# Optimization experiments

Hardware: AMD Instinct MI355X
Metric: run time of the kernel (lower is better)

The kernel has to match this reference:

```python
import jax, jax.numpy as jnp
import numpy as np

N_WIRES = 8
DIM = 2 ** N_WIRES  # 256 amplitudes
# PauliZ sign table: Z_SIGNS[w, i] = +1 if bit w of basis index i is 0 else -1
_bits = (np.arange(DIM)[None, :] >> (N_WIRES - 1 - np.arange(N_WIRES))[:, None]) & 1
Z_SIGNS = jnp.asarray(1.0 - 2.0 * _bits, dtype=jnp.float32)  # [8, 256]


def quantum_project(t, theta):
    """Batched 8-wire circuit: RX(x_w) encoder + trainable RX(theta_w) (RX gates on the
    same wire compose additively), then CNOT ring, then <Z_w> for each wire.
    t: [B, S, E] -> returns [B, S, H, 8]."""
    B, S, E = t.shape
    H = E // N_WIRES
    ang = (t.reshape(B, S, H, N_WIRES) + theta) * 0.5  # RX(a)RX(b)=RX(a+b)
    q0 = jnp.cos(ang).astype(jnp.complex64)
    q1 = (-1j * jnp.sin(ang)).astype(jnp.complex64)
    # Build product state |psi> = \otimes_w [cos(a_w/2), -i sin(a_w/2)] -> [B,S,H,256]
    state = jnp.ones((B, S, H, 1), jnp.complex64)
    for w in range(N_WIRES):
        qb = jnp.stack([q0[..., w], q1[..., w]], axis=-1)  # [B,S,H,2]
        state = (state[..., :, None] * qb[..., None, :]).reshape(B, S, H, -1)
    state = state.reshape((B, S, H) + (2,) * N_WIRES)  # wire w on axis 3+w
    # CNOT chain 0->1,...,6->7 then ring-closing 7->0
    for cw, tw in [(w, w + 1) for w in range(N_WIRES - 1)] + [(N_WIRES - 1, 0)]:
        s0 = jax.lax.index_in_dim(state, 0, axis=3 + cw, keepdims=True)
        s1 = jnp.flip(jax.lax.index_in_dim(state, 1, axis=3 + cw, keepdims=True), axis=3 + tw)
        state = jnp.concatenate([s0, s1], axis=3 + cw)
    amps = state.reshape(B, S, H, DIM)
    probs = amps.real * amps.real + amps.imag * amps.imag  # [B,S,H,256] float32
    return jnp.einsum('bshd,wd->bshw', probs, Z_SIGNS)  # <Z_w> per wire


def setup_inputs() -> dict:
    key = jax.random.key(0)
    kx, kq, kk, kv, ko, kt = jax.random.split(key, 6)
    B, S, E = 16, 512, 64
    scale = 1.0 / np.sqrt(E)
    return {
        'x': jax.random.normal(kx, (B, S, E), dtype=jnp.float32),
        'Wq': jax.random.normal(kq, (E, E), dtype=jnp.float32) * scale,
        'Wk': jax.random.normal(kk, (E, E), dtype=jnp.float32) * scale,
        'Wv': jax.random.normal(kv, (E, E), dtype=jnp.float32) * scale,
        'Wo': jax.random.normal(ko, (E, E), dtype=jnp.float32) * scale,
        'theta': jax.random.uniform(kt, (N_WIRES,), dtype=jnp.float32, minval=0.0, maxval=2.0 * np.pi),
    }


def reference(x, Wq, Wk, Wv, Wo, theta):
    B, S, E = x.shape
    q = quantum_project(x @ Wq.T, theta)  # [B,S,H,8]
    k = quantum_project(x @ Wk.T, theta)
    v = quantum_project(x @ Wv.T, theta)
    # NOTE: original code never transposes heads to dim 1, so attention mixes HEADS
    # per token: scores [B,S,H,H]. Faithfully reproduced. d_k = 8.
    scores = jnp.einsum('bsiw,bsjw->bsij', q, k) / jnp.float32(np.sqrt(N_WIRES))
    attn = jax.nn.softmax(scores, axis=-1)  # dropout is identity in eval
    out = jnp.einsum('bsij,bsjw->bsiw', attn, v)  # [B,S,H,8]
    # original: out.transpose(1,2).contiguous().view(B,-1,E) -> scrambled layout
    out = out.transpose(0, 2, 1, 3).reshape(B, -1, E)
    return out @ Wo.T
```

## Files before the change

### kernel.cpp

```cpp
#include <hip/hip_runtime.h>


#define WT  4096
#define SPS 66
#define SCS 17

__device__ __forceinline__ float rl(float v, int l) {
    return __int_as_float(__builtin_amdgcn_readlane(__float_as_int(v), l));
}

#define DPP_SHR_STEP(d, j, sh)                                                 \
    {                                                                          \
        float _t = __int_as_float(__builtin_amdgcn_update_dpp(                 \
            0x3f800000, __float_as_int(d), 0x110 + sh, 0xf, 0xf, false));      \
        d *= ((j) >= (sh)) ? _t : 1.0f;                                        \
    }

__device__ __forceinline__ float fastcos(float x) { return __cosf(x); }

__global__ __launch_bounds__(256, 2)
void qattn_fused(const float* __restrict__ xg,
                 const float* __restrict__ wqg, const float* __restrict__ wkg,
                 const float* __restrict__ wvg, const float* __restrict__ wog,
                 const float* __restrict__ thg,
                 float* __restrict__ outg)
{
    __shared__ float sWt[3 * WT];
    __shared__ float sP[4 * 3 * 4 * SPS];
    __shared__ float sScr[64 * SCS];

    const int tid  = threadIdx.x;
    const int lane = tid & 63;
    const int wg   = tid >> 6;
    const int j    = lane & 7;
    const int b    = blockIdx.x >> 5;
    const int grp  = blockIdx.x & 31;

    {
        const float* gm[3] = {wqg, wkg, wvg};
        #pragma unroll
        for (int m = 0; m < 3; ++m) {
            #pragma unroll
            for (int r = 0; r < 4; ++r) {
                const int g = tid + 256 * r;
                const float4 v = ((const float4*)gm[m])[g];
                const int e = g >> 4, kq = g & 15;
                const int c0 = (2 * e + 4 * kq) & 127;
                const int c1 = (c0 + 2) & 127;
                *(float2*)&sWt[m * WT + 256 * kq + c0]       = make_float2(v.x, v.y);
                *(float2*)&sWt[m * WT + 256 * kq + 128 + c1] = make_float2(v.z, v.w);
            }
        }
    }
    float xr[4];
    {
        const float* xb = xg + ((size_t)(b * 512 + grp * 16 + wg * 4)) * 64 + lane;
        xr[0] = xb[0]; xr[1] = xb[64]; xr[2] = xb[128]; xr[3] = xb[192];
    }
    const float thf = thg[j];
    __syncthreads();

    {
        float acc[3][4];
        #pragma unroll
        for (int m = 0; m < 3; ++m)
            #pragma unroll
            for (int t = 0; t < 4; ++t) acc[m][t] = 0.f;

        #pragma unroll 8
        for (int kk = 0; kk < 32; ++kk) {
            const int col = (2 * lane + 2 * kk) & 127;
            const float2 wq = *(const float2*)&sWt[0 * WT + kk * 128 + col];
            const float2 wk = *(const float2*)&sWt[1 * WT + kk * 128 + col];
            const float2 wv = *(const float2*)&sWt[2 * WT + kk * 128 + col];
            #pragma unroll
            for (int t = 0; t < 4; ++t) {
                const float x0 = rl(xr[t], 2 * kk);
                const float x1 = rl(xr[t], 2 * kk + 1);
                acc[0][t] = fmaf(wq.x, x0, fmaf(wq.y, x1, acc[0][t]));
                acc[1][t] = fmaf(wk.x, x0, fmaf(wk.y, x1, acc[1][t]));
                acc[2][t] = fmaf(wv.x, x0, fmaf(wv.y, x1, acc[2][t]));
            }
        }
        #pragma unroll
        for (int m = 0; m < 3; ++m) {
            #pragma unroll
            for (int t = 0; t < 4; ++t) {
                const float c = fastcos(acc[m][t] + thf);
                float d = c;
                DPP_SHR_STEP(d, j, 1)
                DPP_SHR_STEP(d, j, 2)
                DPP_SHR_STEP(d, j, 4)
                float ex = (j == 0) ? 1.0f : c;
                DPP_SHR_STEP(ex, j, 1)
                DPP_SHR_STEP(ex, j, 2)
                DPP_SHR_STEP(ex, j, 4)
                const int base = (((wg * 3 + m) * 4 + t)) * SPS + lane;
                if (j > 0)  sP[base]     = d;
                if (j == 7) sP[base - 7] = ex;
            }
        }
    }
    __syncthreads();

    if (wg < 2) {
        const int tg = wg * 8 + (lane >> 3);
        const int i  = lane & 7;
        const int qb = (((tg >> 2) * 3 + 0) * 4 + (tg & 3)) * SPS;
        const int kb = qb + 4 * SPS;
        const int vb = qb + 8 * SPS;
        float q[8];
        #pragma unroll
        for (int c = 0; c < 4; ++c)
            *(float2*)&q[2 * c] = *(const float2*)&sP[qb + 8 * i + 2 * c];
        float p[8];
        float sum = 0.f;
        #pragma unroll
        for (int jj = 0; jj < 8; ++jj) {
            float kv[8];
            #pragma unroll
            for (int c = 0; c < 4; ++c)
                *(float2*)&kv[2 * c] = *(const float2*)&sP[kb + 8 * jj + 2 * c];
            float s = q[0] * kv[0];
            #pragma unroll
            for (int w = 1; w < 8; ++w) s = fmaf(q[w], kv[w], s);
            p[jj] = __expf(s * 0.35355339059327373f);
            sum += p[jj];
        }
        const float rinv = 1.0f / sum;
        float o[8];
        #pragma unroll
        for (int w = 0; w < 8; ++w) o[w] = 0.f;
        #pragma unroll
        for (int jj = 0; jj < 8; ++jj) {
            float vv[8];
            #pragma unroll
            for (int c = 0; c < 4; ++c)
                *(float2*)&vv[2 * c] = *(const float2*)&sP[vb + 8 * jj + 2 * c];
            const float a = p[jj] * rinv;
            #pragma unroll
            for (int w = 0; w < 8; ++w) o[w] = fmaf(a, vv[w], o[w]);
        }
        const int rho = i * 2 + (tg >> 3);
        const int cb  = 8 * (tg & 7);
        #pragma unroll
        for (int w = 0; w < 8; ++w) sScr[(cb + w) * SCS + rho] = o[w];
    } else {
        const int lt = tid & 127;
        #pragma unroll
        for (int r = 0; r < 8; ++r) {
            const int g = lt + 128 * r;
            const float4 v = ((const float4*)wog)[g];
            const int e = g >> 4, kq = g & 15;
            const int c0 = (2 * e + 4 * kq) & 127;
            const int c1 = (c0 + 2) & 127;
            *(float2*)&sWt[256 * kq + c0]       = make_float2(v.x, v.y);
            *(float2*)&sWt[256 * kq + 128 + c1] = make_float2(v.z, v.w);
        }
    }
    __syncthreads();

    {
        float wo[64];
        #pragma unroll
        for (int kk = 0; kk < 32; ++kk) {
            const int col = (2 * lane + 2 * kk) & 127;
            const float2 w2 = *(const float2*)&sWt[kk * 128 + col];
            wo[2 * kk] = w2.x; wo[2 * kk + 1] = w2.y;
        }
        #pragma unroll
        for (int rr = 0; rr < 4; ++rr) {
            const int rho = wg * 4 + rr;
            const float sv = sScr[lane * SCS + rho];
            float y0 = 0.f, y1 = 0.f, y2 = 0.f, y3 = 0.f;
            #pragma unroll
            for (int k = 0; k < 64; k += 4) {
                y0 = fmaf(wo[k],     rl(sv, k),     y0);
                y1 = fmaf(wo[k + 1], rl(sv, k + 1), y1);
                y2 = fmaf(wo[k + 2], rl(sv, k + 2), y2);
                y3 = fmaf(wo[k + 3], rl(sv, k + 3), y3);
            }
            const float y = (y0 + y1) + (y2 + y3);
            const int head = rho >> 1, oct = rho & 1;
            outg[((size_t)(b * 512 + head * 64 + grp * 2 + oct)) * 64 + lane] = y;
        }
    }
}

extern "C" void kernel_launch(void* const* d_in, const int* in_sizes, int n_in,
                              void* d_out, int out_size, void* d_ws, size_t ws_size,
                              hipStream_t stream) {
    const float* x  = (const float*)d_in[0];
    const float* wq = (const float*)d_in[1];
    const float* wk = (const float*)d_in[2];
    const float* wv = (const float*)d_in[3];
    const float* wo = (const float*)d_in[4];
    const float* th = (const float*)d_in[5];
    float* out = (float*)d_out;
    qattn_fused<<<dim3(512), dim3(256), 0, stream>>>(x, wq, wk, wv, wo, th, out);
}
```

Measured before the change: 73.50 us.

## Broadcast activations via LDS float4 reads instead of readlane, pad weight layout

Stages the block's x tile in shared memory and reads it as broadcast float4 loads, replacing per-element readlane broadcasts in the QKV projection. The output projection does the same, reading attention rows from a row-major padded scratch buffer. Weights are stored transposed with a padded row stride to avoid bank conflicts, replacing the earlier swizzle. This trades scalar readlane work for extra LDS traffic and LDS footprint.

```diff
diff --git a/kernel.cpp b/kernel.cpp
--- a/kernel.cpp
+++ b/kernel.cpp
@@ -1,13 +1,10 @@
 #include <hip/hip_runtime.h>
 
 
-#define WT  4096
+#define PS  130
+#define WTM (32 * PS)
 #define SPS 66
-#define SCS 17
-
-__device__ __forceinline__ float rl(float v, int l) {
-    return __int_as_float(__builtin_amdgcn_readlane(__float_as_int(v), l));
-}
+#define SCS 68
 
 #define DPP_SHR_STEP(d, j, sh)                                                 \
     {                                                                          \
@@ -15,8 +12,6 @@
             0x3f800000, __float_as_int(d), 0x110 + sh, 0xf, 0xf, false));      \
         d *= ((j) >= (sh)) ? _t : 1.0f;                                        \
     }
-
-__device__ __forceinline__ float fastcos(float x) { return __cosf(x); }
 
 __global__ __launch_bounds__(256, 2)
 void qattn_fused(const float* __restrict__ xg,
@@ -25,9 +20,10 @@
                  const float* __restrict__ thg,
                  float* __restrict__ outg)
 {
-    __shared__ float sWt[3 * WT];
-    __shared__ float sP[4 * 3 * 4 * SPS];
-    __shared__ float sScr[64 * SCS];
+    __shared__ float sWt[3 * WTM];
+    __shared__ __align__(16) float sX[16 * 64];
+    __shared__ float sP[48 * SPS];
+    __shared__ __align__(16) float sScr[16 * SCS];
 
     const int tid  = threadIdx.x;
     const int lane = tid & 63;
@@ -45,17 +41,14 @@
                 const int g = tid + 256 * r;
                 const float4 v = ((const float4*)gm[m])[g];
                 const int e = g >> 4, kq = g & 15;
-                const int c0 = (2 * e + 4 * kq) & 127;
-                const int c1 = (c0 + 2) & 127;
-                *(float2*)&sWt[m * WT + 256 * kq + c0]       = make_float2(v.x, v.y);
-                *(float2*)&sWt[m * WT + 256 * kq + 128 + c1] = make_float2(v.z, v.w);
-            }
-        }
-    }
-    float xr[4];
-    {
-        const float* xb = xg + ((size_t)(b * 512 + grp * 16 + wg * 4)) * 64 + lane;
-        xr[0] = xb[0]; xr[1] = xb[64]; xr[2] = xb[128]; xr[3] = xb[192];
+                *(float2*)&sWt[m * WTM + (2 * kq) * PS + 2 * e]     = make_float2(v.x, v.y);
+                *(float2*)&sWt[m * WTM + (2 * kq + 1) * PS + 2 * e] = make_float2(v.z, v.w);
+            }
+        }
+    }
+    {
+        const float4 xv = ((const float4*)(xg + (size_t)(b * 512 + grp * 16) * 64))[tid];
+        *(float4*)&sX[tid * 4] = xv;
     }
     const float thf = thg[j];
     __syncthreads();
@@ -67,26 +60,38 @@
             #pragma unroll
             for (int t = 0; t < 4; ++t) acc[m][t] = 0.f;
 
-        #pragma unroll 8
-        for (int kk = 0; kk < 32; ++kk) {
-            const int col = (2 * lane + 2 * kk) & 127;
-            const float2 wq = *(const float2*)&sWt[0 * WT + kk * 128 + col];
-            const float2 wk = *(const float2*)&sWt[1 * WT + kk * 128 + col];
-            const float2 wv = *(const float2*)&sWt[2 * WT + kk * 128 + col];
+        const float* w0 = &sWt[0 * WTM + 2 * lane];
+        const float* w1 = &sWt[1 * WTM + 2 * lane];
+        const float* w2 = &sWt[2 * WTM + 2 * lane];
+        const float* xb0 = &sX[(wg * 4) * 64];
+
+        #pragma unroll
+        for (int kk2 = 0; kk2 < 16; ++kk2) {
+            float4 xt[4];
+            #pragma unroll
+            for (int t = 0; t < 4; ++t)
+                xt[t] = *(const float4*)(xb0 + t * 64 + kk2 * 4);
+            const float2 qA = *(const float2*)(w0 + (2 * kk2) * PS);
+            const float2 qB = *(const float2*)(w0 + (2 * kk2 + 1) * PS);
+            const float2 kA = *(const float2*)(w1 + (2 * kk2) * PS);
+            const float2 kB = *(const float2*)(w1 + (2 * kk2 + 1) * PS);
+            const float2 vA = *(const float2*)(w2 + (2 * kk2) * PS);
+            const float2 vB = *(const float2*)(w2 + (2 * kk2 + 1) * PS);
             #pragma unroll
             for (int t = 0; t < 4; ++t) {
-                const float x0 = rl(xr[t], 2 * kk);
-                const float x1 = rl(xr[t], 2 * kk + 1);
-                acc[0][t] = fmaf(wq.x, x0, fmaf(wq.y, x1, acc[0][t]));
-                acc[1][t] = fmaf(wk.x, x0, fmaf(wk.y, x1, acc[1][t]));
-                acc[2][t] = fmaf(wv.x, x0, fmaf(wv.y, x1, acc[2][t]));
+                acc[0][t] = fmaf(qA.x, xt[t].x, fmaf(qA.y, xt[t].y, acc[0][t]));
+                acc[0][t] = fmaf(qB.x, xt[t].z, fmaf(qB.y, xt[t].w, acc[0][t]));
+                acc[1][t] = fmaf(kA.x, xt[t].x, fmaf(kA.y, xt[t].y, acc[1][t]));
+                acc[1][t] = fmaf(kB.x, xt[t].z, fmaf(kB.y, xt[t].w, acc[1][t]));
+                acc[2][t] = fmaf(vA.x, xt[t].x, fmaf(vA.y, xt[t].y, acc[2][t]));
+                acc[2][t] = fmaf(vB.x, xt[t].z, fmaf(vB.y, xt[t].w, acc[2][t]));
             }
         }
         #pragma unroll
         for (int m = 0; m < 3; ++m) {
             #pragma unroll
             for (int t = 0; t < 4; ++t) {
-                const float c = fastcos(acc[m][t] + thf);
+                const float c = __cosf(acc[m][t] + thf);
                 float d = c;
                 DPP_SHR_STEP(d, j, 1)
                 DPP_SHR_STEP(d, j, 2)
@@ -95,7 +100,7 @@
                 DPP_SHR_STEP(ex, j, 1)
                 DPP_SHR_STEP(ex, j, 2)
                 DPP_SHR_STEP(ex, j, 4)
-                const int base = (((wg * 3 + m) * 4 + t)) * SPS + lane;
+                const int base = ((wg * 3 + m) * 4 + t) * SPS + lane;
                 if (j > 0)  sP[base]     = d;
                 if (j == 7) sP[base - 7] = ex;
             }
@@ -141,10 +146,9 @@
             #pragma unroll
             for (int w = 0; w < 8; ++w) o[w] = fmaf(a, vv[w], o[w]);
         }
-        const int rho = i * 2 + (tg >> 3);
-        const int cb  = 8 * (tg & 7);
-        #pragma unroll
-        for (int w = 0; w < 8; ++w) sScr[(cb + w) * SCS + rho] = o[w];
+        float* sd = &sScr[(i * 2 + (tg >> 3)) * SCS + 8 * (tg & 7)];
+        *(float4*)sd       = make_float4(o[0], o[1], o[2], o[3]);
+        *(float4*)(sd + 4) = make_float4(o[4], o[5], o[6], o[7]);
     } else {
         const int lt = tid & 127;
         #pragma unroll
@@ -152,10 +156,8 @@
             const int g = lt + 128 * r;
             const float4 v = ((const float4*)wog)[g];
             const int e = g >> 4, kq = g & 15;
-            const int c0 = (2 * e + 4 * kq) & 127;
-            const int c1 = (c0 + 2) & 127;
-            *(float2*)&sWt[256 * kq + c0]       = make_float2(v.x, v.y);
-            *(float2*)&sWt[256 * kq + 128 + c1] = make_float2(v.z, v.w);
+            *(float2*)&sWt[(2 * kq) * PS + 2 * e]     = make_float2(v.x, v.y);
+            *(float2*)&sWt[(2 * kq + 1) * PS + 2 * e] = make_float2(v.z, v.w);
         }
     }
     __syncthreads();
@@ -164,21 +166,20 @@
         float wo[64];
         #pragma unroll
         for (int kk = 0; kk < 32; ++kk) {
-            const int col = (2 * lane + 2 * kk) & 127;
-            const float2 w2 = *(const float2*)&sWt[kk * 128 + col];
-            wo[2 * kk] = w2.x; wo[2 * kk + 1] = w2.y;
+            const float2 w2v = *(const float2*)&sWt[kk * PS + 2 * lane];
+            wo[2 * kk] = w2v.x; wo[2 * kk + 1] = w2v.y;
         }
         #pragma unroll
         for (int rr = 0; rr < 4; ++rr) {
             const int rho = wg * 4 + rr;
-            const float sv = sScr[lane * SCS + rho];
             float y0 = 0.f, y1 = 0.f, y2 = 0.f, y3 = 0.f;
             #pragma unroll
-            for (int k = 0; k < 64; k += 4) {
-                y0 = fmaf(wo[k],     rl(sv, k),     y0);
-                y1 = fmaf(wo[k + 1], rl(sv, k + 1), y1);
-                y2 = fmaf(wo[k + 2], rl(sv, k + 2), y2);
-                y3 = fmaf(wo[k + 3], rl(sv, k + 3), y3);
+            for (int q4 = 0; q4 < 16; ++q4) {
+                const float4 sv = *(const float4*)&sScr[rho * SCS + q4 * 4];
+                y0 = fmaf(wo[4 * q4],     sv.x, y0);
+                y1 = fmaf(wo[4 * q4 + 1], sv.y, y1);
+                y2 = fmaf(wo[4 * q4 + 2], sv.z, y2);
+                y3 = fmaf(wo[4 * q4 + 3], sv.w, y3);
             }
             const float y = (y0 + y1) + (y2 + y3);
             const int head = rho >> 1, oct = rho & 1;
```

Measured after the change: 124.1 us. 68.8% more time.

## Run per-warp attention in all waves and load Wo directly from global

Applied to the files above, without the earlier changes.

Each wave now computes attention only on its own four tokens' projections, so the block-wide barrier between the projection and attention stages is removed and all four waves do attention work instead of two. The Wo staging into shared memory is dropped; each lane reads its Wo row straight from global memory into registers. The shared-memory layouts are padded and aligned so Q/K/V reads and scratch writes can use float4 accesses. The risks are redundant work, since half the lanes compute duplicate attention results, and uncoalesced per-lane global reads of Wo.

```diff
diff --git a/kernel.cpp b/kernel.cpp
--- a/kernel.cpp
+++ b/kernel.cpp
@@ -2,12 +2,8 @@
 
 
 #define WT  4096
-#define SPS 66
-#define SCS 17
-
-__device__ __forceinline__ float rl(float v, int l) {
-    return __int_as_float(__builtin_amdgcn_readlane(__float_as_int(v), l));
-}
+#define SPS 68
+#define SCS 68
 
 #define DPP_SHR_STEP(d, j, sh)                                                 \
     {                                                                          \
@@ -16,7 +12,9 @@
         d *= ((j) >= (sh)) ? _t : 1.0f;                                        \
     }
 
-__device__ __forceinline__ float fastcos(float x) { return __cosf(x); }
+__device__ __forceinline__ float rl(float v, int l) {
+    return __int_as_float(__builtin_amdgcn_readlane(__float_as_int(v), l));
+}
 
 __global__ __launch_bounds__(256, 2)
 void qattn_fused(const float* __restrict__ xg,
@@ -26,8 +24,8 @@
                  float* __restrict__ outg)
 {
     __shared__ float sWt[3 * WT];
-    __shared__ float sP[4 * 3 * 4 * SPS];
-    __shared__ float sScr[64 * SCS];
+    __shared__ __align__(16) float sP[48 * SPS];
+    __shared__ __align__(16) float sScr[16 * SCS];
 
     const int tid  = threadIdx.x;
     const int lane = tid & 63;
@@ -86,7 +84,7 @@
         for (int m = 0; m < 3; ++m) {
             #pragma unroll
             for (int t = 0; t < 4; ++t) {
-                const float c = fastcos(acc[m][t] + thf);
+                const float c = __cosf(acc[m][t] + thf);
                 float d = c;
                 DPP_SHR_STEP(d, j, 1)
                 DPP_SHR_STEP(d, j, 2)
@@ -95,35 +93,34 @@
                 DPP_SHR_STEP(ex, j, 1)
                 DPP_SHR_STEP(ex, j, 2)
                 DPP_SHR_STEP(ex, j, 4)
-                const int base = (((wg * 3 + m) * 4 + t)) * SPS + lane;
+                const int base = ((wg * 3 + m) * 4 + t) * SPS + lane;
                 if (j > 0)  sP[base]     = d;
                 if (j == 7) sP[base - 7] = ex;
             }
         }
     }
-    __syncthreads();
 
-    if (wg < 2) {
-        const int tg = wg * 8 + (lane >> 3);
-        const int i  = lane & 7;
-        const int qb = (((tg >> 2) * 3 + 0) * 4 + (tg & 3)) * SPS;
-        const int kb = qb + 4 * SPS;
-        const int vb = qb + 8 * SPS;
+    {
+        const int t  = lane >> 4;
+        const int i  = j;
+        const int tt = wg * 4 + t;
+        const int qb = ((wg * 3 + 0) * 4 + t) * SPS;
+        const int kb = ((wg * 3 + 1) * 4 + t) * SPS;
+        const int vb = ((wg * 3 + 2) * 4 + t) * SPS;
         float q[8];
-        #pragma unroll
-        for (int c = 0; c < 4; ++c)
-            *(float2*)&q[2 * c] = *(const float2*)&sP[qb + 8 * i + 2 * c];
+        *(float4*)&q[0] = *(const float4*)&sP[qb + 8 * i];
+        *(float4*)&q[4] = *(const float4*)&sP[qb + 8 * i + 4];
         float p[8];
         float sum = 0.f;
         #pragma unroll
         for (int jj = 0; jj < 8; ++jj) {
-            float kv[8];
-            #pragma unroll
-            for (int c = 0; c < 4; ++c)
-                *(float2*)&kv[2 * c] = *(const float2*)&sP[kb + 8 * jj + 2 * c];
-            float s = q[0] * kv[0];
-            #pragma unroll
-            for (int w = 1; w < 8; ++w) s = fmaf(q[w], kv[w], s);
+            const float4 k0 = *(const float4*)&sP[kb + 8 * jj];
+            const float4 k1 = *(const float4*)&sP[kb + 8 * jj + 4];
+            float s = q[0] * k0.x;
+            s = fmaf(q[1], k0.y, s); s = fmaf(q[2], k0.z, s);
+            s = fmaf(q[3], k0.w, s); s = fmaf(q[4], k1.x, s);
+            s = fmaf(q[5], k1.y, s); s = fmaf(q[6], k1.z, s);
+            s = fmaf(q[7], k1.w, s);
             p[jj] = __expf(s * 0.35355339059327373f);
             sum += p[jj];
         }
@@ -133,29 +130,18 @@
         for (int w = 0; w < 8; ++w) o[w] = 0.f;
         #pragma unroll
         for (int jj = 0; jj < 8; ++jj) {
-            float vv[8];
-            #pragma unroll
-            for (int c = 0; c < 4; ++c)
-                *(float2*)&vv[2 * c] = *(const float2*)&sP[vb + 8 * jj + 2 * c];
+            const float4 v0 = *(const float4*)&sP[vb + 8 * jj];
+            const float4 v1 = *(const float4*)&sP[vb + 8 * jj + 4];
             const float a = p[jj] * rinv;
-            #pragma unroll
-            for (int w = 0; w < 8; ++w) o[w] = fmaf(a, vv[w], o[w]);
+            o[0] = fmaf(a, v0.x, o[0]); o[1] = fmaf(a, v0.y, o[1]);
+            o[2] = fmaf(a, v0.z, o[2]); o[3] = fmaf(a, v0.w, o[3]);
+            o[4] = fmaf(a, v1.x, o[4]); o[5] = fmaf(a, v1.y, o[5]);
+            o[6] = fmaf(a, v1.z, o[6]); o[7] = fmaf(a, v1.w, o[7]);
         }
-        const int rho = i * 2 + (tg >> 3);
-        const int cb  = 8 * (tg & 7);
-        #pragma unroll
-        for (int w = 0; w < 8; ++w) sScr[(cb + w) * SCS + rho] = o[w];
-    } else {
-        const int lt = tid & 127;
-        #pragma unroll
-        for (int r = 0; r < 8; ++r) {
-            const int g = lt + 128 * r;
-            const float4 v = ((const float4*)wog)[g];
-            const int e = g >> 4, kq = g & 15;
-            const int c0 = (2 * e + 4 * kq) & 127;
-            const int c1 = (c0 + 2) & 127;
-            *(float2*)&sWt[256 * kq + c0]       = make_float2(v.x, v.y);
-            *(float2*)&sWt[256 * kq + 128 + c1] = make_float2(v.z, v.w);
+        if (!(lane & 8)) {
+            float* sd = &sScr[(i * 2 + (tt >> 3)) * SCS + 8 * (tt & 7)];
+            *(float4*)sd       = make_float4(o[0], o[1], o[2], o[3]);
+            *(float4*)(sd + 4) = make_float4(o[4], o[5], o[6], o[7]);
         }
     }
     __syncthreads();
@@ -163,15 +149,15 @@
     {
         float wo[64];
         #pragma unroll
-        for (int kk = 0; kk < 32; ++kk) {
-            const int col = (2 * lane + 2 * kk) & 127;
-            const float2 w2 = *(const float2*)&sWt[kk * 128 + col];
-            wo[2 * kk] = w2.x; wo[2 * kk + 1] = w2.y;
+        for (int kc = 0; kc < 16; ++kc) {
+            const float4 v = *(const float4*)(wog + lane * 64 + kc * 4);
+            wo[4 * kc] = v.x; wo[4 * kc + 1] = v.y;
+            wo[4 * kc + 2] = v.z; wo[4 * kc + 3] = v.w;
         }
         #pragma unroll
         for (int rr = 0; rr < 4; ++rr) {
             const int rho = wg * 4 + rr;
-            const float sv = sScr[lane * SCS + rho];
+            const float sv = sScr[rho * SCS + lane];
             float y0 = 0.f, y1 = 0.f, y2 = 0.f, y3 = 0.f;
             #pragma unroll
             for (int k = 0; k < 64; k += 4) {
```

New measurement: 75.28 us. +2.4%, slower.
